# Optimization experiments

Hardware: AMD Instinct MI355X
Metric: run time of the kernel (lower is better)

The kernel has to match this reference:

```python
import jax, jax.numpy as jnp
import numpy as np

T, B, L = 4, 8192, 50
VOCAB, D = 100000, 128


def setup_inputs() -> dict:
    key = jax.random.key(0)
    ks = jax.random.split(key, 10)
    inp = {
        "indices": jax.random.randint(ks[0], (T, B, L), 0, VOCAB, dtype=jnp.int32),
        "lengths": jax.random.randint(ks[1], (T, B), 0, L, dtype=jnp.int32),
        "tables": jax.random.normal(ks[2], (T, VOCAB, D), dtype=jnp.float32) * 0.02,
        "W1": jax.random.normal(ks[3], (D, D), dtype=jnp.float32) * (1.0 / np.sqrt(D)),
        "b1": jax.random.normal(ks[4], (D,), dtype=jnp.float32) * 0.01,
        "W2": jax.random.normal(ks[5], (D, D), dtype=jnp.float32) * (1.0 / np.sqrt(D)),
        "b2": jax.random.normal(ks[6], (D,), dtype=jnp.float32) * 0.01,
        "W3": jax.random.normal(ks[7], (D, D), dtype=jnp.float32) * (1.0 / np.sqrt(D)),
        "b3": jax.random.normal(ks[8], (D,), dtype=jnp.float32) * 0.01,
    }
    return inp


def reference(indices, lengths, tables, W1, b1, W2, b2, W3, b3):
    # Per-table jagged gather + SUM pooling (EmbeddingBagCollection default).
    t, b, l = indices.shape
    emb = jax.vmap(lambda tab, idx: tab[idx])(tables, indices)  # [T,B,L,D]
    mask = (jnp.arange(l, dtype=lengths.dtype) < lengths[..., None])[..., None]
    pooled = jnp.sum(jnp.where(mask, emb, jnp.zeros((), emb.dtype)), axis=2)  # [T,B,D]
    # torch.cat over dict values concatenates along dim 0 -> [T*B, D]
    x = pooled.reshape(t * b, -1)
    # nn.Sequential of three Linear(D, D) layers, no activation
    x = x @ W1.T + b1
    x = x @ W2.T + b2
    x = x @ W3.T + b3
    return x
```

## Files before the change

kernel.cpp:

```cpp
#include <hip/hip_runtime.h>


#define T_ 4
#define B_ 8192
#define L_ 50
#define VOCAB_ 100000
#define D_ 128
#define ROWS 8
#define NBAGS (T_ * B_)

#define WS_M  0
#define WS_C  16384

__global__ __launch_bounds__(128) void combine(const float* __restrict__ W1,
                                               const float* __restrict__ W2,
                                               const float* __restrict__ W3,
                                               const float* __restrict__ b1,
                                               const float* __restrict__ b2,
                                               const float* __restrict__ b3,
                                               float* __restrict__ ws) {
  __shared__ float a1[D_];
  const int j = threadIdx.x;
  const int i = blockIdx.x;
  if (i < D_) {
    float acc = 0.f;
    for (int k = 0; k < D_; ++k)
      acc += W1[k * D_ + i] * W2[j * D_ + k];
    a1[j] = acc;
    __syncthreads();
    float m = 0.f;
    for (int k = 0; k < D_; ++k)
      m += a1[k] * W3[j * D_ + k];
    ws[WS_M + i * D_ + j] = m;
  } else {
    float c1 = b2[j];
    for (int k = 0; k < D_; ++k)
      c1 += b1[k] * W2[j * D_ + k];
    a1[j] = c1;
    __syncthreads();
    float c = b3[j];
    for (int k = 0; k < D_; ++k)
      c += a1[k] * W3[j * D_ + k];
    ws[WS_C + j] = c;
  }
}

__global__ __launch_bounds__(256) void fused(const int* __restrict__ indices,
                                             const int* __restrict__ lengths,
                                             const float* __restrict__ tables,
                                             const float* __restrict__ ws,
                                             float* __restrict__ out) {
  __shared__ __align__(16) float pooled_sh[ROWS][D_];
  __shared__ int idx_sh[ROWS][L_];
  __shared__ int len_sh[ROWS];
  __shared__ int bag_ctr;

  const int tid = threadIdx.x;
  const int g0  = blockIdx.x * ROWS;

  if (tid == 0) bag_ctr = 0;
  for (int k = tid; k < ROWS * L_; k += 256)
    idx_sh[k / L_][k % L_] = indices[g0 * L_ + k];
  if (tid < ROWS) len_sh[tid] = lengths[g0 + tid];
  __syncthreads();

  {
    const int lane = tid & 63;
    const int d0   = lane * 2;
    const int t    = g0 >> 13;
    const float* __restrict__ tab = tables + (size_t)t * (VOCAB_ * D_) + d0;

    for (;;) {
      int pos = 0;
      if (lane == 0) pos = atomicAdd(&bag_ctr, 1);
      pos = __shfl(pos, 0, 64);
      if (pos >= ROWS) break;
      const int len = len_sh[pos];
      const int* __restrict__ il = idx_sh[pos];
      float ax = 0.f, ay = 0.f;
      int l = 0;
      for (; l + 7 < len; l += 8) {
        const int i0 = il[l + 0], i1 = il[l + 1], i2 = il[l + 2], i3 = il[l + 3];
        const int i4 = il[l + 4], i5 = il[l + 5], i6 = il[l + 6], i7 = il[l + 7];
        const float2 v0 = *(const float2*)(tab + (size_t)i0 * D_);
        const float2 v1 = *(const float2*)(tab + (size_t)i1 * D_);
        const float2 v2 = *(const float2*)(tab + (size_t)i2 * D_);
        const float2 v3 = *(const float2*)(tab + (size_t)i3 * D_);
        const float2 v4 = *(const float2*)(tab + (size_t)i4 * D_);
        const float2 v5 = *(const float2*)(tab + (size_t)i5 * D_);
        const float2 v6 = *(const float2*)(tab + (size_t)i6 * D_);
        const float2 v7 = *(const float2*)(tab + (size_t)i7 * D_);
        ax += v0.x; ay += v0.y;  ax += v1.x; ay += v1.y;
        ax += v2.x; ay += v2.y;  ax += v3.x; ay += v3.y;
        ax += v4.x; ay += v4.y;  ax += v5.x; ay += v5.y;
        ax += v6.x; ay += v6.y;  ax += v7.x; ay += v7.y;
      }
      for (; l + 1 < len; l += 2) {
        const float2 va = *(const float2*)(tab + (size_t)il[l] * D_);
        const float2 vb = *(const float2*)(tab + (size_t)il[l + 1] * D_);
        ax += va.x; ay += va.y;  ax += vb.x; ay += vb.y;
      }
      if (l < len) {
        const float2 v = *(const float2*)(tab + (size_t)il[l] * D_);
        ax += v.x; ay += v.y;
      }
      *(float2*)&pooled_sh[pos][d0] = make_float2(ax, ay);
    }
  }
  __syncthreads();

  const int j  = tid & (D_ - 1);
  const int rh = (tid >> 7) * 4;
  const float* __restrict__ Mg = ws + WS_M;
  const float cj = ws[WS_C + j];
  float acc0 = cj, acc1 = cj, acc2 = cj, acc3 = cj;
#pragma unroll 4
  for (int i = 0; i < D_; ++i) {
    const float m = Mg[i * D_ + j];
    acc0 += pooled_sh[rh + 0][i] * m;
    acc1 += pooled_sh[rh + 1][i] * m;
    acc2 += pooled_sh[rh + 2][i] * m;
    acc3 += pooled_sh[rh + 3][i] * m;
  }
  out[(size_t)(g0 + rh + 0) * D_ + j] = acc0;
  out[(size_t)(g0 + rh + 1) * D_ + j] = acc1;
  out[(size_t)(g0 + rh + 2) * D_ + j] = acc2;
  out[(size_t)(g0 + rh + 3) * D_ + j] = acc3;
}

extern "C" void kernel_launch(void* const* d_in, const int* in_sizes, int n_in,
                              void* d_out, int out_size, void* d_ws, size_t ws_size,
                              hipStream_t stream) {
  const int*   indices = (const int*)d_in[0];
  const int*   lengths = (const int*)d_in[1];
  const float* tables  = (const float*)d_in[2];
  const float* W1      = (const float*)d_in[3];
  const float* b1      = (const float*)d_in[4];
  const float* W2      = (const float*)d_in[5];
  const float* b2      = (const float*)d_in[6];
  const float* W3      = (const float*)d_in[7];
  const float* b3      = (const float*)d_in[8];
  float*       out     = (float*)d_out;
  float*       ws      = (float*)d_ws;

  combine<<<D_ + 1, D_, 0, stream>>>(W1, W2, W3, b1, b2, b3, ws);
  fused<<<NBAGS / ROWS, 256, 0, stream>>>(indices, lengths, tables, ws, out);
}
```

Before: 344.6 us.

## Gather rows with float4 half-wave split and precomputed byte offsets, 16 bags per block

Each wave now splits a bag between two half-waves, each fetching alternate rows with 16-byte float4 loads, and combines them with a cross-half shuffle. Indices are pre-shifted into byte offsets in shared memory, which removes the 64-bit multiply per row. The block handles 16 bags instead of 8, with an occupancy hint, and the GEMV epilogue is rewritten to produce float2 outputs per thread over 16 rows. This aims to improve gather memory-level parallelism and to amortize loading the combined weight matrix, at the cost of halving the grid and adding shuffle overhead.

```diff
diff --git a/kernel.cpp b/kernel.cpp
--- a/kernel.cpp
+++ b/kernel.cpp
@@ -6,7 +6,7 @@
 #define L_ 50
 #define VOCAB_ 100000
 #define D_ 128
-#define ROWS 8
+#define ROWS 16
 #define NBAGS (T_ * B_)
 
 #define WS_M  0
@@ -45,13 +45,13 @@
   }
 }
 
-__global__ __launch_bounds__(256) void fused(const int* __restrict__ indices,
-                                             const int* __restrict__ lengths,
-                                             const float* __restrict__ tables,
-                                             const float* __restrict__ ws,
-                                             float* __restrict__ out) {
+__global__ __launch_bounds__(256, 8) void fused(const int* __restrict__ indices,
+                                                const int* __restrict__ lengths,
+                                                const float* __restrict__ tables,
+                                                const float* __restrict__ ws,
+                                                float* __restrict__ out) {
   __shared__ __align__(16) float pooled_sh[ROWS][D_];
-  __shared__ int idx_sh[ROWS][L_];
+  __shared__ int off_sh[ROWS][L_];
   __shared__ int len_sh[ROWS];
   __shared__ int bag_ctr;
 
@@ -60,15 +60,17 @@
 
   if (tid == 0) bag_ctr = 0;
   for (int k = tid; k < ROWS * L_; k += 256)
-    idx_sh[k / L_][k % L_] = indices[g0 * L_ + k];
+    off_sh[k / L_][k % L_] = indices[g0 * L_ + k] << 9;
   if (tid < ROWS) len_sh[tid] = lengths[g0 + tid];
   __syncthreads();
 
   {
     const int lane = tid & 63;
-    const int d0   = lane * 2;
+    const int half = lane >> 5;
+    const int d0   = (lane & 31) * 4;
     const int t    = g0 >> 13;
-    const float* __restrict__ tab = tables + (size_t)t * (VOCAB_ * D_) + d0;
+    const char* __restrict__ tab =
+        (const char*)(tables + (size_t)t * (VOCAB_ * D_) + d0);
 
     for (;;) {
       int pos = 0;
@@ -76,56 +78,62 @@
       pos = __shfl(pos, 0, 64);
       if (pos >= ROWS) break;
       const int len = len_sh[pos];
-      const int* __restrict__ il = idx_sh[pos];
-      float ax = 0.f, ay = 0.f;
+      const int* __restrict__ il = off_sh[pos];
+      float ax = 0.f, ay = 0.f, az = 0.f, aw = 0.f;
       int l = 0;
       for (; l + 7 < len; l += 8) {
-        const int i0 = il[l + 0], i1 = il[l + 1], i2 = il[l + 2], i3 = il[l + 3];
-        const int i4 = il[l + 4], i5 = il[l + 5], i6 = il[l + 6], i7 = il[l + 7];
-        const float2 v0 = *(const float2*)(tab + (size_t)i0 * D_);
-        const float2 v1 = *(const float2*)(tab + (size_t)i1 * D_);
-        const float2 v2 = *(const float2*)(tab + (size_t)i2 * D_);
-        const float2 v3 = *(const float2*)(tab + (size_t)i3 * D_);
-        const float2 v4 = *(const float2*)(tab + (size_t)i4 * D_);
-        const float2 v5 = *(const float2*)(tab + (size_t)i5 * D_);
-        const float2 v6 = *(const float2*)(tab + (size_t)i6 * D_);
-        const float2 v7 = *(const float2*)(tab + (size_t)i7 * D_);
-        ax += v0.x; ay += v0.y;  ax += v1.x; ay += v1.y;
-        ax += v2.x; ay += v2.y;  ax += v3.x; ay += v3.y;
-        ax += v4.x; ay += v4.y;  ax += v5.x; ay += v5.y;
-        ax += v6.x; ay += v6.y;  ax += v7.x; ay += v7.y;
+        const int o0 = il[l + 0 + half];
+        const int o1 = il[l + 2 + half];
+        const int o2 = il[l + 4 + half];
+        const int o3 = il[l + 6 + half];
+        const float4 v0 = *(const float4*)(tab + o0);
+        const float4 v1 = *(const float4*)(tab + o1);
+        const float4 v2 = *(const float4*)(tab + o2);
+        const float4 v3 = *(const float4*)(tab + o3);
+        ax += v0.x; ay += v0.y; az += v0.z; aw += v0.w;
+        ax += v1.x; ay += v1.y; az += v1.z; aw += v1.w;
+        ax += v2.x; ay += v2.y; az += v2.z; aw += v2.w;
+        ax += v3.x; ay += v3.y; az += v3.z; aw += v3.w;
       }
       for (; l + 1 < len; l += 2) {
-        const float2 va = *(const float2*)(tab + (size_t)il[l] * D_);
-        const float2 vb = *(const float2*)(tab + (size_t)il[l + 1] * D_);
-        ax += va.x; ay += va.y;  ax += vb.x; ay += vb.y;
+        const float4 v = *(const float4*)(tab + il[l + half]);
+        ax += v.x; ay += v.y; az += v.z; aw += v.w;
       }
-      if (l < len) {
-        const float2 v = *(const float2*)(tab + (size_t)il[l] * D_);
-        ax += v.x; ay += v.y;
+      if (l < len && half == 0) {
+        const float4 v = *(const float4*)(tab + il[l]);
+        ax += v.x; ay += v.y; az += v.z; aw += v.w;
       }
-      *(float2*)&pooled_sh[pos][d0] = make_float2(ax, ay);
+      ax += __shfl_xor(ax, 32, 64);
+      ay += __shfl_xor(ay, 32, 64);
+      az += __shfl_xor(az, 32, 64);
+      aw += __shfl_xor(aw, 32, 64);
+      if (half == 0)
+        *(float4*)&pooled_sh[pos][d0] = make_float4(ax, ay, az, aw);
     }
   }
   __syncthreads();
 
-  const int j  = tid & (D_ - 1);
-  const int rh = (tid >> 7) * 4;
+  const int jc = (tid & 63) * 2;
+  const int rh = (tid >> 6) * 4;
   const float* __restrict__ Mg = ws + WS_M;
-  const float cj = ws[WS_C + j];
-  float acc0 = cj, acc1 = cj, acc2 = cj, acc3 = cj;
+  const float2 c2 = *(const float2*)(ws + WS_C + jc);
+  float2 a0 = c2, a1 = c2, a2 = c2, a3 = c2;
 #pragma unroll 4
   for (int i = 0; i < D_; ++i) {
-    const float m = Mg[i * D_ + j];
-    acc0 += pooled_sh[rh + 0][i] * m;
-    acc1 += pooled_sh[rh + 1][i] * m;
-    acc2 += pooled_sh[rh + 2][i] * m;
-    acc3 += pooled_sh[rh + 3][i] * m;
+    const float2 m = *(const float2*)(Mg + i * D_ + jc);
+    const float p0 = pooled_sh[rh + 0][i];
+    const float p1 = pooled_sh[rh + 1][i];
+    const float p2 = pooled_sh[rh + 2][i];
+    const float p3 = pooled_sh[rh + 3][i];
+    a0.x += p0 * m.x; a0.y += p0 * m.y;
+    a1.x += p1 * m.x; a1.y += p1 * m.y;
+    a2.x += p2 * m.x; a2.y += p2 * m.y;
+    a3.x += p3 * m.x; a3.y += p3 * m.y;
   }
-  out[(size_t)(g0 + rh + 0) * D_ + j] = acc0;
-  out[(size_t)(g0 + rh + 1) * D_ + j] = acc1;
-  out[(size_t)(g0 + rh + 2) * D_ + j] = acc2;
-  out[(size_t)(g0 + rh + 3) * D_ + j] = acc3;
+  *(float2*)&out[(size_t)(g0 + rh + 0) * D_ + jc] = a0;
+  *(float2*)&out[(size_t)(g0 + rh + 1) * D_ + jc] = a1;
+  *(float2*)&out[(size_t)(g0 + rh + 2) * D_ + jc] = a2;
+  *(float2*)&out[(size_t)(g0 + rh + 3) * D_ + jc] = a3;
 }
 
 extern "C" void kernel_launch(void* const* d_in, const int* in_sizes, int n_in,
```

Result: no change. 348.8 us (+1.2%).
